# Kernel optimization log

Measured on AMD Instinct MI355X. Metric: run time of the kernel, lower is better.

The kernel has to match this reference:

```python
import jax, jax.numpy as jnp
import numpy as np

B, N_REG, D_IN = 32, 116, 256
N_NODES = B * N_REG            # 3712
E_PER_G = N_REG * 10           # avg degree 10
E = B * E_PER_G                # 37120
HEADS = 8
HID = [256, 128, 64]
D_OUT = 256
LN_EPS = 1e-5


def _layer_norm(x, scale, bias):
    mu = x.mean(-1, keepdims=True)
    var = ((x - mu) ** 2).mean(-1, keepdims=True)
    return (x - mu) * jax.lax.rsqrt(var + LN_EPS) * scale + bias


def _gat_layer(x, W, b, a_src, a_dst, src, dst, concat):
    """PyG-style GATConv (shared lin, self-loops, leaky_relu 0.2) + ELU + LayerNorm."""
    N = x.shape[0]
    H, C = a_src.shape
    h = (x @ W).reshape(N, H, C)                      # (N, H, C)
    sl = jnp.arange(N, dtype=src.dtype)               # self-loops (PyG default)
    s = jnp.concatenate([src, sl])
    d = jnp.concatenate([dst, sl])
    al = (h * a_src).sum(-1)                          # (N, H)
    ar = (h * a_dst).sum(-1)                          # (N, H)
    e = jax.nn.leaky_relu(al[s] + ar[d], 0.2)         # (E', H)
    m = jax.ops.segment_max(e, d, num_segments=N)
    ex = jnp.exp(e - m[d])
    den = jax.ops.segment_sum(ex, d, num_segments=N)
    alpha = ex / den[d]                               # segment softmax over incoming edges
    out = jax.ops.segment_sum(h[s] * alpha[..., None], d, num_segments=N)  # (N, H, C)
    out = out.reshape(N, H * C) if concat else out.mean(1)
    return out + b


def setup_inputs() -> dict:
    key = jax.random.key(0)
    ks = list(jax.random.split(key, 32))
    node_features = jax.random.normal(ks[0], (N_NODES, D_IN), dtype=jnp.float32)
    # edges: random within each graph (disconnected batched graph)
    off = (jnp.arange(B, dtype=jnp.int32) * N_REG)[:, None]
    src = (jax.random.randint(ks[1], (B, E_PER_G), 0, N_REG, dtype=jnp.int32) + off).reshape(-1)
    dst = (jax.random.randint(ks[2], (B, E_PER_G), 0, N_REG, dtype=jnp.int32) + off).reshape(-1)
    batch = jnp.repeat(jnp.arange(B, dtype=jnp.int32), N_REG)

    def lin(k, fin, fout):
        s = 1.0 / np.sqrt(fin)
        return jax.random.uniform(k, (fin, fout), jnp.float32, -s, s)

    dims_in = [D_IN, HID[0] * HEADS, HID[1] * HEADS]
    p = {}
    ki = 3
    for i, (fin, c) in enumerate(zip(dims_in, HID)):
        concat = i < len(HID) - 1
        wdim = c * HEADS
        p[f"w{i}"] = lin(ks[ki], fin, wdim); ki += 1
        p[f"b{i}"] = jnp.zeros((wdim if concat else c,), jnp.float32)
        p[f"as{i}"] = jax.random.normal(ks[ki], (HEADS, c), jnp.float32) * 0.1; ki += 1
        p[f"ad{i}"] = jax.random.normal(ks[ki], (HEADS, c), jnp.float32) * 0.1; ki += 1
        ldim = wdim if concat else c
        p[f"ls{i}"] = jnp.ones((ldim,), jnp.float32)
        p[f"lb{i}"] = jnp.zeros((ldim,), jnp.float32)
    p["wp"] = lin(ks[ki], HID[-1], D_OUT); ki += 1
    p["bp"] = jnp.zeros((D_OUT,), jnp.float32)
    p["lsp"] = jnp.ones((D_OUT,), jnp.float32)
    p["lbp"] = jnp.zeros((D_OUT,), jnp.float32)
    p["wq"] = lin(ks[ki], D_OUT, 1); ki += 1
    p["bq"] = jnp.zeros((1,), jnp.float32)
    return dict(node_features=node_features, src=src, dst=dst, batch=batch, **p)


def reference(node_features, src, dst, batch,
              w0, b0, as0, ad0, ls0, lb0,
              w1, b1, as1, ad1, ls1, lb1,
              w2, b2, as2, ad2, ls2, lb2,
              wp, bp, lsp, lbp, wq, bq):
    x = node_features
    x = _layer_norm(jax.nn.elu(_gat_layer(x, w0, b0, as0, ad0, src, dst, True)), ls0, lb0)
    x = _layer_norm(jax.nn.elu(_gat_layer(x, w1, b1, as1, ad1, src, dst, True)), ls1, lb1)
    x = _layer_norm(jax.nn.elu(_gat_layer(x, w2, b2, as2, ad2, src, dst, False)), ls2, lb2)
    node_out = jax.nn.gelu(_layer_norm(x @ wp + bp, lsp, lbp), approximate=False)  # (N, 256)
    pool_w = jax.nn.softmax(node_out @ wq + bq, axis=0)                            # (N, 1) global softmax
    num = jax.ops.segment_sum(node_out * pool_w, batch, num_segments=B)            # (B, 256)
    den = jnp.maximum(jax.ops.segment_sum(pool_w, batch, num_segments=B), 1e-8)    # (B, 1)
    graph_features = num / den
    return graph_features, node_out
```

## Files before the change

### kernel.cpp

```cpp
#include <hip/hip_runtime.h>
#include <hip/hip_bf16.h>
#include <math.h>

typedef __hip_bfloat16 bf16;
typedef short short8 __attribute__((ext_vector_type(8)));
typedef float f32x4 __attribute__((ext_vector_type(4)));

__device__ __forceinline__ float b2f(const bf16 v) { return __bfloat162float(v); }
__device__ __forceinline__ bf16 f2b(const float v) { return __float2bfloat16(v); }

__device__ __forceinline__ float bits2f(short s) {
  unsigned u = ((unsigned)(unsigned short)s) << 16;
  float f;
  __builtin_memcpy(&f, &u, 4);
  return f;
}
__device__ __forceinline__ short f2bits(float f) {
  bf16 b = f2b(f);
  short s;
  __builtin_memcpy(&s, &b, 2);
  return s;
}

__device__ __forceinline__ float ldsel(const void* p, size_t i, int f32) {
  return f32 ? ((const float*)p)[i] : b2f(((const bf16*)p)[i]);
}
__device__ __forceinline__ void stsel(void* p, size_t i, float v, int f32) {
  if (f32) ((float*)p)[i] = v; else ((bf16*)p)[i] = f2b(v);
}

__device__ __forceinline__ void load8f(const void* p, int idx, int f32, float* o) {
  if (f32) {
    const float4* q = (const float4*)((const float*)p + idx);
    float4 a = q[0], b = q[1];
    o[0] = a.x; o[1] = a.y; o[2] = a.z; o[3] = a.w;
    o[4] = b.x; o[5] = b.y; o[6] = b.z; o[7] = b.w;
  } else {
    union { short8 v; short s[8]; } u;
    u.v = *(const short8*)((const bf16*)p + idx);
#pragma unroll
    for (int j = 0; j < 8; ++j) o[j] = bits2f(u.s[j]);
  }
}

#define NN 3712
#define NE 37120
#define NG 32
#define NREG 116
#define MAXDEG 48


__global__ __launch_bounds__(256) void k_detect(const void* nf, const void* w0, int* flags) {
  __shared__ int bad[2];
  if (threadIdx.x < 2) bad[threadIdx.x] = 0;
  __syncthreads();
  const bf16* a = (const bf16*)nf;
  const bf16* b = (const bf16*)w0;
  int l0 = 0, l1 = 0;
  for (int i = threadIdx.x; i < 4096; i += 256) {
    float x = b2f(a[i]); if (!(fabsf(x) < 1e4f)) l0++;
    float y = b2f(b[i]); if (!(fabsf(y) < 1e4f)) l1++;
  }
  if (l0) atomicAdd(&bad[0], l0);
  if (l1) atomicAdd(&bad[1], l1);
  __syncthreads();
  if (threadIdx.x == 0) { flags[0] = bad[0] > 0; flags[1] = bad[1] > 0; }
}

__global__ __launch_bounds__(256) void k_zero(int* __restrict__ p, int n) {
  int i = blockIdx.x * 256 + threadIdx.x;
  if (i < n) p[i] = 0;
}

__global__ __launch_bounds__(256) void k_scatter(const int* __restrict__ src, const int* __restrict__ dst,
                                                 int* __restrict__ cnt, int* __restrict__ bucket, int E) {
  int e = blockIdx.x * 256 + threadIdx.x;
  if (e < E) {
    int d = dst[e], s = src[e];
    if ((unsigned)d < NN && (unsigned)s < NN) {
      int p = atomicAdd(&cnt[d], 1);
      if (p < MAXDEG) bucket[d * MAXDEG + p] = s;
    }
  }
}

__global__ __launch_bounds__(256) void k_tox0(const void* __restrict__ in, bf16* __restrict__ out,
                                              const int* __restrict__ flags) {
  int f = flags[0];
  int bid = blockIdx.x;
  int n = (bid & 7) * 464 + (bid >> 3);
  int i = n * 256 + threadIdx.x;
  out[i] = f2b(ldsel(in, i, f));
}

__global__ __launch_bounds__(256) void k_transpose(const void* __restrict__ W, bf16* __restrict__ Wt,
                                                   int K, int N, const int* __restrict__ flags) {
  int f = flags[1];
  __shared__ float tile[32][33];
  int tx = threadIdx.x & 31, ty = threadIdx.x >> 5;
  int k0 = blockIdx.x * 32, n0 = blockIdx.y * 32;
#pragma unroll
  for (int i = 0; i < 4; ++i)
    tile[ty + i * 8][tx] = ldsel(W, (size_t)(k0 + ty + i * 8) * N + n0 + tx, f);
  __syncthreads();
#pragma unroll
  for (int i = 0; i < 4; ++i)
    Wt[(size_t)(n0 + ty + i * 8) * K + k0 + tx] = f2b(tile[tx][ty + i * 8]);
}

__global__ __launch_bounds__(256) void k_gemm_mfma(const bf16* __restrict__ A, const bf16* __restrict__ Bt,
                                                   bf16* __restrict__ C, int M, int N, int K) {
  __shared__ short As[64 * 72];
  __shared__ short Bs[64 * 72];
  int tid = threadIdx.x;
  int wave = tid >> 6, lane = tid & 63;
  int wr = wave >> 1, wc = wave & 1;
  int quad = lane >> 4, ml = lane & 15;

  int nbx = N >> 6;
  int total = gridDim.x;
  int id = blockIdx.x;
  int tile = ((total & 7) == 0) ? ((id & 7) * (total >> 3) + (id >> 3)) : id;
  int n0 = (tile % nbx) << 6;
  int m0 = (tile / nbx) << 6;

  f32x4 acc[2][2];
#pragma unroll
  for (int rt = 0; rt < 2; ++rt)
#pragma unroll
    for (int ct = 0; ct < 2; ++ct)
#pragma unroll
      for (int r = 0; r < 4; ++r) acc[rt][ct][r] = 0.f;

  for (int k0 = 0; k0 < K; k0 += 64) {
    __syncthreads();
#pragma unroll
    for (int i = 0; i < 2; ++i) {
      int c = tid + (i << 8);
      int row = c >> 3, kg = (c & 7) << 3;
      *(uint4*)&As[row * 72 + kg] = *(const uint4*)&A[(size_t)(m0 + row) * K + k0 + kg];
      *(uint4*)&Bs[row * 72 + kg] = *(const uint4*)&Bt[(size_t)(n0 + row) * K + k0 + kg];
    }
    __syncthreads();
    short8 af[2][2], bfr[2][2];
#pragma unroll
    for (int rt = 0; rt < 2; ++rt)
#pragma unroll
      for (int kk = 0; kk < 2; ++kk)
        af[rt][kk] = *(const short8*)&As[(wr * 32 + rt * 16 + ml) * 72 + kk * 32 + quad * 8];
#pragma unroll
    for (int ct = 0; ct < 2; ++ct)
#pragma unroll
      for (int kk = 0; kk < 2; ++kk)
        bfr[ct][kk] = *(const short8*)&Bs[(wc * 32 + ct * 16 + ml) * 72 + kk * 32 + quad * 8];
#pragma unroll
    for (int rt = 0; rt < 2; ++rt)
#pragma unroll
      for (int ct = 0; ct < 2; ++ct)
#pragma unroll
        for (int kk = 0; kk < 2; ++kk)
          acc[rt][ct] = __builtin_amdgcn_mfma_f32_16x16x32_bf16(af[rt][kk], bfr[ct][kk], acc[rt][ct], 0, 0, 0);
  }
#pragma unroll
  for (int rt = 0; rt < 2; ++rt)
#pragma unroll
    for (int ct = 0; ct < 2; ++ct)
#pragma unroll
      for (int r = 0; r < 4; ++r) {
        int grow = m0 + wr * 32 + rt * 16 + quad * 4 + r;
        int gcol = n0 + wc * 32 + ct * 16 + ml;
        C[(size_t)grow * N + gcol] = f2b(acc[rt][ct][r]);
      }
}

__global__ void k_attn(const bf16* __restrict__ H, const void* __restrict__ a_s,
                       const void* __restrict__ a_d, float* __restrict__ al,
                       float* __restrict__ ar, int C, const int* __restrict__ flags) {
  int wF = flags[1];
  int t = threadIdx.x;
  int D = 8 * C;
  int i0 = t * 8;
  int bid = blockIdx.x;
  int nb = (bid & 7) * 58 + (bid >> 3);
  float as8[8], ad8[8];
  load8f(a_s, i0, wF, as8);
  load8f(a_d, i0, wF, ad8);
  int G = C >> 3;
  int hd = i0 / C;
  for (int it = 0; it < 8; ++it) {
    int n = nb * 8 + it;
    union { short8 v; short s[8]; } u;
    u.v = *(const short8*)&H[(size_t)n * D + i0];
    float ps = 0.f, pd = 0.f;
#pragma unroll
    for (int j = 0; j < 8; ++j) {
      float h = bits2f(u.s[j]);
      ps = fmaf(h, as8[j], ps);
      pd = fmaf(h, ad8[j], pd);
    }
    for (int off = G >> 1; off; off >>= 1) {
      ps += __shfl_xor(ps, off);
      pd += __shfl_xor(pd, off);
    }
    if ((t & (G - 1)) == 0) {
      al[n * 8 + hd] = ps;
      ar[n * 8 + hd] = pd;
    }
  }
}

__global__ __launch_bounds__(256) void k_edgew(const float* __restrict__ al, const float* __restrict__ ar,
                                               const int* __restrict__ cnt, const int* __restrict__ bucket,
                                               float* __restrict__ mbuf, float* __restrict__ ibuf) {
  int t = threadIdx.x;
  int q = t >> 6, l = t & 63, hd = l >> 3, el = l & 7;
  int bid = blockIdx.x;
  int d = (bid & 7) * 464 + (bid >> 3) * 4 + q;
  int deg = cnt[d]; deg = deg > MAXDEG ? MAXDEG : deg;
  int total = deg + 1;
  float ard = ar[d * 8 + hd];
  float lgv[7];
  float m = -1e30f;
#pragma unroll
  for (int k = 0; k < 7; ++k) {
    int e = el + k * 8;
    float lg = -1e30f;
    if (e < total) {
      int s = e < deg ? bucket[d * MAXDEG + e] : d;
      lg = al[s * 8 + hd] + ard;
      lg = lg > 0.f ? lg : 0.2f * lg;
    }
    lgv[k] = lg;
    m = fmaxf(m, lg);
  }
#pragma unroll
  for (int off = 4; off; off >>= 1) m = fmaxf(m, __shfl_xor(m, off));
  float den = 0.f;
#pragma unroll
  for (int k = 0; k < 7; ++k) den += (lgv[k] > -1e29f) ? expf(lgv[k] - m) : 0.f;
#pragma unroll
  for (int off = 4; off; off >>= 1) den += __shfl_xor(den, off);
  if (el == 0) { mbuf[d * 8 + hd] = m; ibuf[d * 8 + hd] = 1.f / den; }
}

template<int C>
__global__ __launch_bounds__(256, 1) void k_aggm(const bf16* __restrict__ H,
    const float* __restrict__ al, const float* __restrict__ ar,
    const float* __restrict__ mbuf, const float* __restrict__ ibuf,
    const int* __restrict__ cnt, const int* __restrict__ bucket,
    bf16* __restrict__ Y) {
  constexpr int D = 8 * C;
  constexpr int KP = 136;
  __shared__ short P[128 * KP];
  __shared__ short Ht[C * KP];
  int t = threadIdx.x;
  int bid = blockIdx.x;
  int x = bid & 7, j = bid >> 3;
  int g = x * 4 + (j & 3);
  int h = j >> 2;
  int gbase = g * NREG;

  short8 z = {0, 0, 0, 0, 0, 0, 0, 0};
  for (int i = t; i < 128 * KP / 8; i += 256) *(short8*)&P[i * 8] = z;
  for (int i = t; i < C * KP / 8; i += 256) *(short8*)&Ht[i * 8] = z;
  __syncthreads();

  constexpr int CH = C / 8;
  for (int idx = t; idx < NREG * CH; idx += 256) {
    int s = idx / CH, c0 = (idx % CH) * 8;
    union { short8 v; short x2[8]; } u;
    u.v = *(const short8*)&H[(size_t)(gbase + s) * D + h * C + c0];
#pragma unroll
    for (int jj = 0; jj < 8; ++jj) Ht[(c0 + jj) * KP + s] = u.x2[jj];
  }
  if (t < NREG) {
    int gd = gbase + t;
    int deg = cnt[gd]; deg = deg > MAXDEG ? MAXDEG : deg;
    int total = deg + 1;
    float ard = ar[gd * 8 + h];
    float mm = mbuf[gd * 8 + h], inv = ibuf[gd * 8 + h];
    for (int base = 0; base < total; base += 8) {
      int sg[8]; float av[8];
#pragma unroll
      for (int jj = 0; jj < 8; ++jj) {
        int e = base + jj;
        sg[jj] = (e < deg) ? bucket[gd * MAXDEG + e] : gd;
      }
#pragma unroll
      for (int jj = 0; jj < 8; ++jj) av[jj] = al[sg[jj] * 8 + h];
#pragma unroll
      for (int jj = 0; jj < 8; ++jj) {
        if (base + jj < total) {
          float lg = av[jj] + ard;
          lg = lg > 0.f ? lg : 0.2f * lg;
          float alpha = expf(lg - mm) * inv;
          int off = t * KP + (sg[jj] - gbase);
          P[off] = f2bits(bits2f(P[off]) + alpha);
        }
      }
    }
  }
  __syncthreads();

  constexpr int CT = C / 32;
  int wave = t >> 6, lane = t & 63;
  int wr = wave >> 1, wc = wave & 1;
  int quad = lane >> 4, ml = lane & 15;
  f32x4 acc[4][CT];
#pragma unroll
  for (int a = 0; a < 4; ++a)
#pragma unroll
    for (int b = 0; b < CT; ++b)
#pragma unroll
      for (int r = 0; r < 4; ++r) acc[a][b][r] = 0.f;
#pragma unroll
  for (int ks = 0; ks < 4; ++ks) {
    short8 af[4], bf8[CT];
#pragma unroll
    for (int rt = 0; rt < 4; ++rt)
      af[rt] = *(const short8*)&P[(wr * 64 + rt * 16 + ml) * KP + ks * 32 + quad * 8];
#pragma unroll
    for (int ct = 0; ct < CT; ++ct)
      bf8[ct] = *(const short8*)&Ht[(wc * (C / 2) + ct * 16 + ml) * KP + ks * 32 + quad * 8];
#pragma unroll
    for (int rt = 0; rt < 4; ++rt)
#pragma unroll
      for (int ct = 0; ct < CT; ++ct)
        acc[rt][ct] = __builtin_amdgcn_mfma_f32_16x16x32_bf16(af[rt], bf8[ct], acc[rt][ct], 0, 0, 0);
  }
#pragma unroll
  for (int rt = 0; rt < 4; ++rt) {
    int m = wr * 64 + rt * 16 + quad * 4;
#pragma unroll
    for (int r = 0; r < 4; ++r) {
      if (m + r < NREG) {
#pragma unroll
        for (int ct = 0; ct < CT; ++ct) {
          int n = wc * (C / 2) + ct * 16 + ml;
          Y[(size_t)(gbase + m + r) * D + h * C + n] = f2b(acc[rt][ct][r]);
        }
      }
    }
  }
}

template<int D>
__global__ __launch_bounds__(256) void k_ln(bf16* __restrict__ X, const void* __restrict__ bias,
                                            const void* __restrict__ ls, const void* __restrict__ lb,
                                            const int* __restrict__ flags) {
  int wF = flags[1];
  constexpr int VPT = D / 256;
  int t = threadIdx.x;
  int bid = blockIdx.x;
  int nb = (bid & 7) * 58 + (bid >> 3);
  int node = nb * 8 + (t >> 5);
  int l32 = t & 31;
  float v[VPT * 8];
  float s1 = 0.f, s2 = 0.f;
#pragma unroll
  for (int j = 0; j < VPT; ++j) {
    int c0 = (l32 + j * 32) * 8;
    union { short8 u; short x[8]; } uu;
    uu.u = *(const short8*)&X[(size_t)node * D + c0];
    float bb[8];
    load8f(bias, c0, wF, bb);
#pragma unroll
    for (int k = 0; k < 8; ++k) {
      float vv = bits2f(uu.x[k]) + bb[k];
      vv = vv > 0.f ? vv : expf(vv) - 1.f;
      v[j * 8 + k] = vv; s1 += vv; s2 += vv * vv;
    }
  }
#pragma unroll
  for (int off = 16; off; off >>= 1) { s1 += __shfl_xor(s1, off); s2 += __shfl_xor(s2, off); }
  float mu = s1 / D;
  float rs = rsqrtf(s2 / D - mu * mu + 1e-5f);
#pragma unroll
  for (int j = 0; j < VPT; ++j) {
    int c0 = (l32 + j * 32) * 8;
    float g8[8], b8[8];
    load8f(ls, c0, wF, g8);
    load8f(lb, c0, wF, b8);
    union { short8 u; short x[8]; } uu;
#pragma unroll
    for (int k = 0; k < 8; ++k)
      uu.x[k] = f2bits((v[j * 8 + k] - mu) * rs * g8[k] + b8[k]);
    *(short8*)&X[(size_t)node * D + c0] = uu.u;
  }
}

__global__ void k_agg(const bf16* __restrict__ H, const float* __restrict__ al,
                      const float* __restrict__ ar, const float* __restrict__ mbuf,
                      const float* __restrict__ ibuf, const int* __restrict__ cnt,
                      const int* __restrict__ bucket, const void* __restrict__ bias,
                      const void* __restrict__ ls, const void* __restrict__ lb,
                      bf16* __restrict__ Xout, int C, int concat,
                      const int* __restrict__ flags) {
  int wF = flags[1];
  int bid = blockIdx.x;
  int d = (bid & 7) * 464 + (bid >> 3);
  int t = threadIdx.x;
  int D = 8 * C;
  __shared__ int sid[MAXDEG + 4];
  __shared__ float vals[512];

  int deg = cnt[d]; deg = deg > MAXDEG ? MAXDEG : deg;
  int total = deg + 1;
  int padded = (total + 3) & ~3;
  if (t < padded) sid[t] = t < deg ? bucket[d * MAXDEG + t] : d;
  __syncthreads();

  int i0 = t * 8;
  int hd = i0 / C;
  float m = mbuf[d * 8 + hd], inv = ibuf[d * 8 + hd], ard = ar[d * 8 + hd];

  float acc[8] = {0.f, 0.f, 0.f, 0.f, 0.f, 0.f, 0.f, 0.f};
  const bf16* __restrict__ Hp = H + i0;
  for (int eb = 0; eb < padded; eb += 4) {
    int s4[4]; float a4[4]; short8 u4[4];
#pragma unroll
    for (int j = 0; j < 4; ++j) s4[j] = sid[eb + j];
#pragma unroll
    for (int j = 0; j < 4; ++j) {
      a4[j] = al[s4[j] * 8 + hd];
      u4[j] = *(const short8*)&Hp[(size_t)s4[j] * D];
    }
#pragma unroll
    for (int j = 0; j < 4; ++j) {
      float lg = a4[j] + ard;
      lg = lg > 0.f ? lg : 0.2f * lg;
      float we = (eb + j) < total ? expf(lg - m) * inv : 0.f;
      union { short8 v; short s[8]; } uu; uu.v = u4[j];
#pragma unroll
      for (int k2 = 0; k2 < 8; ++k2) acc[k2] = fmaf(we, bits2f(uu.s[k2]), acc[k2]);
    }
  }

#pragma unroll
  for (int j = 0; j < 8; ++j) vals[i0 + j] = acc[j];
  __syncthreads();
  float v = 0.f;
#pragma unroll
  for (int h = 0; h < 8; ++h) v += vals[h * 64 + t];
  v = v * 0.125f + ldsel(bias, t, wF);
  v = v > 0.f ? v : expf(v) - 1.f;
  float s1 = v, s2 = v * v;
#pragma unroll
  for (int off = 32; off; off >>= 1) { s1 += __shfl_xor(s1, off); s2 += __shfl_xor(s2, off); }
  float mu = s1 * (1.f / 64.f);
  float var = s2 * (1.f / 64.f) - mu * mu;
  float rs = rsqrtf(var + 1e-5f);
  Xout[(size_t)d * 64 + t] = f2b((v - mu) * rs * ldsel(ls, t, wF) + ldsel(lb, t, wF));
}

__global__ __launch_bounds__(256) void k_proj(const bf16* __restrict__ X3, const void* __restrict__ wp,
                                              const void* __restrict__ bp, const void* __restrict__ lsp,
                                              const void* __restrict__ lbp, const void* __restrict__ wq,
                                              const void* __restrict__ bq,
                                              float* __restrict__ q, void* __restrict__ dout,
                                              const int* __restrict__ flags) {
  int wF = flags[1], xF = flags[0];
  int bid = blockIdx.x;
  int n = (bid & 7) * 464 + (bid >> 3);
  int t = threadIdx.x;
  int lane = t & 63, wave = t >> 6;
  __shared__ float xs[64];
  __shared__ float r1[4], r2[4];
  __shared__ float sMu, sRs;
  if (t < 64) xs[t] = b2f(X3[n * 64 + t]);
  __syncthreads();
  float y = ldsel(bp, t, wF);
#pragma unroll 8
  for (int k = 0; k < 64; ++k) y = fmaf(xs[k], ldsel(wp, k * 256 + t, wF), y);
  float s1 = y, s2 = y * y;
#pragma unroll
  for (int off = 32; off; off >>= 1) { s1 += __shfl_down(s1, off); s2 += __shfl_down(s2, off); }
  if (lane == 0) { r1[wave] = s1; r2[wave] = s2; }
  __syncthreads();
  if (t == 0) {
    float S1 = r1[0] + r1[1] + r1[2] + r1[3];
    float S2 = r2[0] + r2[1] + r2[2] + r2[3];
    float mu = S1 / 256.f;
    sMu = mu; sRs = rsqrtf(S2 / 256.f - mu * mu + 1e-5f);
  }
  __syncthreads();
  float v = (y - sMu) * sRs * ldsel(lsp, t, wF) + ldsel(lbp, t, wF);
  float g = 0.5f * v * (1.f + erff(v * 0.70710678118654752f));
  stsel(dout, (size_t)NG * 256 + (size_t)n * 256 + t, g, xF);
  float qv = g * ldsel(wq, t, wF);
#pragma unroll
  for (int off = 32; off; off >>= 1) qv += __shfl_down(qv, off);
  if (lane == 0) r1[wave] = qv;
  __syncthreads();
  if (t == 0) q[n] = r1[0] + r1[1] + r1[2] + r1[3] + ldsel(bq, 0, wF);
}

__global__ __launch_bounds__(256) void k_pool(void* __restrict__ dout, const float* __restrict__ q,
                                              const int* __restrict__ flags) {
  int xF = flags[0];
  int bid = blockIdx.x;
  int b = (bid & 7) * 4 + (bid >> 3);
  int t = threadIdx.x;
  __shared__ float es[NREG];
  __shared__ float sDen;
  if (t < NREG) es[t] = q[b * NREG + t];
  __syncthreads();
  if (t == 0) {
    float m = -1e30f;
    for (int i = 0; i < NREG; ++i) m = fmaxf(m, es[i]);
    float den = 0.f;
    for (int i = 0; i < NREG; ++i) { float e = expf(es[i] - m); es[i] = e; den += e; }
    sDen = den;
  }
  __syncthreads();
  float acc = 0.f;
  for (int i = 0; i < NREG; ++i)
    acc = fmaf(es[i], ldsel(dout, (size_t)NG * 256 + (size_t)(b * NREG + i) * 256 + t, xF), acc);
  stsel(dout, (size_t)b * 256 + t, acc / sDen, xF);
}

extern "C" void kernel_launch(void* const* d_in, const int* in_sizes, int n_in,
                              void* d_out, int out_size, void* d_ws, size_t ws_size,
                              hipStream_t stream) {
  const void* nf  = d_in[0];
  const int* src  = (const int*)d_in[1];
  const int* dst  = (const int*)d_in[2];
  const void *w0 = d_in[4],  *b0 = d_in[5],  *as0 = d_in[6], *ad0 = d_in[7],  *ls0 = d_in[8],  *lb0 = d_in[9];
  const void *w1 = d_in[10], *b1 = d_in[11], *as1 = d_in[12], *ad1 = d_in[13], *ls1 = d_in[14], *lb1 = d_in[15];
  const void *w2 = d_in[16], *b2 = d_in[17], *as2 = d_in[18], *ad2 = d_in[19], *ls2 = d_in[20], *lb2 = d_in[21];
  const void *wp = d_in[22], *bp = d_in[23], *lsp = d_in[24], *lbp = d_in[25], *wq = d_in[26], *bq = d_in[27];

  int* flags  = (int*)d_ws;
  float* al   = (float*)(flags + 4);
  float* ar   = al + NN * 8;
  int* cnt    = (int*)(ar + NN * 8);
  int* bucket = cnt + NN;
  float* q    = (float*)(bucket + NN * MAXDEG);
  bf16* X     = (bf16*)(q + NN);
  bf16* Hb    = X + (size_t)NN * 2048;

  float* mbuf = (float*)d_out;
  float* ibuf = mbuf + NN * 8;

  bf16* X0  = X;
  bf16* wt0 = X + (1 << 20);
  bf16* wt1 = Hb + (size_t)NN * 1024;
  bf16* wt2 = Hb + (size_t)NN * 512;

  k_detect<<<1, 256, 0, stream>>>(nf, w0, flags);
  k_zero<<<(NN + 255) / 256, 256, 0, stream>>>(cnt, NN);
  k_scatter<<<(NE + 255) / 256, 256, 0, stream>>>(src, dst, cnt, bucket, NE);
  k_tox0<<<NN, 256, 0, stream>>>(nf, X0, flags);

  k_transpose<<<dim3(256 / 32, 2048 / 32), 256, 0, stream>>>(w0, wt0, 256, 2048, flags);
  k_gemm_mfma<<<(2048 / 64) * (NN / 64), 256, 0, stream>>>(X0, wt0, Hb, NN, 2048, 256);
  k_attn<<<NN / 8, 256, 0, stream>>>(Hb, as0, ad0, al, ar, 256, flags);
  k_edgew<<<NN / 4, 256, 0, stream>>>(al, ar, cnt, bucket, mbuf, ibuf);
  k_aggm<256><<<256, 256, 0, stream>>>(Hb, al, ar, mbuf, ibuf, cnt, bucket, X);
  k_ln<2048><<<NN / 8, 256, 0, stream>>>(X, b0, ls0, lb0, flags);

  k_transpose<<<dim3(2048 / 32, 1024 / 32), 256, 0, stream>>>(w1, wt1, 2048, 1024, flags);
  k_gemm_mfma<<<(1024 / 64) * (NN / 64), 256, 0, stream>>>(X, wt1, Hb, NN, 1024, 2048);
  k_attn<<<NN / 8, 128, 0, stream>>>(Hb, as1, ad1, al, ar, 128, flags);
  k_edgew<<<NN / 4, 256, 0, stream>>>(al, ar, cnt, bucket, mbuf, ibuf);
  k_aggm<128><<<256, 256, 0, stream>>>(Hb, al, ar, mbuf, ibuf, cnt, bucket, X);
  k_ln<1024><<<NN / 8, 256, 0, stream>>>(X, b1, ls1, lb1, flags);

  k_transpose<<<dim3(1024 / 32, 512 / 32), 256, 0, stream>>>(w2, wt2, 1024, 512, flags);
  k_gemm_mfma<<<(512 / 64) * (NN / 64), 256, 0, stream>>>(X, wt2, Hb, NN, 512, 1024);
  k_attn<<<NN / 8, 64, 0, stream>>>(Hb, as2, ad2, al, ar, 64, flags);
  k_edgew<<<NN / 4, 256, 0, stream>>>(al, ar, cnt, bucket, mbuf, ibuf);
  k_agg<<<NN, 64, 0, stream>>>(Hb, al, ar, mbuf, ibuf, cnt, bucket, b2, ls2, lb2, X, 64, 0, flags);

  k_proj<<<NN, 256, 0, stream>>>(X, wp, bp, lsp, lbp, wq, bq, q, d_out, flags);
  k_pool<<<NG, 256, 0, stream>>>(d_out, q, flags);
}
```

Measured before the change: 335.4 us.

## Fuse attention logits and edge softmax into per-graph aggregation kernel

Removes the separate k_attn and k_edgew kernels. The per-node source and destination attention logits are now computed inside k_aggm while H is staged into shared memory, using shared-memory atomics, and the per-destination softmax max and denominator are computed in-block from shared memory. The last layer now also uses the MFMA k_aggm<64> path followed by a new mean+ELU+LayerNorm kernel instead of the gather-based k_agg. This saves launches and global round-trips for al/ar/m/inv, in exchange for three serial passes over edges per thread and LDS atomic contention.

Result: slower. 356.1 us (+6.2%).

```diff
diff --git a/kernel.cpp b/kernel.cpp
--- a/kernel.cpp
+++ b/kernel.cpp
@@ -173,86 +173,17 @@
       }
 }
 
-__global__ void k_attn(const bf16* __restrict__ H, const void* __restrict__ a_s,
-                       const void* __restrict__ a_d, float* __restrict__ al,
-                       float* __restrict__ ar, int C, const int* __restrict__ flags) {
-  int wF = flags[1];
-  int t = threadIdx.x;
-  int D = 8 * C;
-  int i0 = t * 8;
-  int bid = blockIdx.x;
-  int nb = (bid & 7) * 58 + (bid >> 3);
-  float as8[8], ad8[8];
-  load8f(a_s, i0, wF, as8);
-  load8f(a_d, i0, wF, ad8);
-  int G = C >> 3;
-  int hd = i0 / C;
-  for (int it = 0; it < 8; ++it) {
-    int n = nb * 8 + it;
-    union { short8 v; short s[8]; } u;
-    u.v = *(const short8*)&H[(size_t)n * D + i0];
-    float ps = 0.f, pd = 0.f;
-#pragma unroll
-    for (int j = 0; j < 8; ++j) {
-      float h = bits2f(u.s[j]);
-      ps = fmaf(h, as8[j], ps);
-      pd = fmaf(h, ad8[j], pd);
-    }
-    for (int off = G >> 1; off; off >>= 1) {
-      ps += __shfl_xor(ps, off);
-      pd += __shfl_xor(pd, off);
-    }
-    if ((t & (G - 1)) == 0) {
-      al[n * 8 + hd] = ps;
-      ar[n * 8 + hd] = pd;
-    }
-  }
-}
-
-__global__ __launch_bounds__(256) void k_edgew(const float* __restrict__ al, const float* __restrict__ ar,
-                                               const int* __restrict__ cnt, const int* __restrict__ bucket,
-                                               float* __restrict__ mbuf, float* __restrict__ ibuf) {
-  int t = threadIdx.x;
-  int q = t >> 6, l = t & 63, hd = l >> 3, el = l & 7;
-  int bid = blockIdx.x;
-  int d = (bid & 7) * 464 + (bid >> 3) * 4 + q;
-  int deg = cnt[d]; deg = deg > MAXDEG ? MAXDEG : deg;
-  int total = deg + 1;
-  float ard = ar[d * 8 + hd];
-  float lgv[7];
-  float m = -1e30f;
-#pragma unroll
-  for (int k = 0; k < 7; ++k) {
-    int e = el + k * 8;
-    float lg = -1e30f;
-    if (e < total) {
-      int s = e < deg ? bucket[d * MAXDEG + e] : d;
-      lg = al[s * 8 + hd] + ard;
-      lg = lg > 0.f ? lg : 0.2f * lg;
-    }
-    lgv[k] = lg;
-    m = fmaxf(m, lg);
-  }
-#pragma unroll
-  for (int off = 4; off; off >>= 1) m = fmaxf(m, __shfl_xor(m, off));
-  float den = 0.f;
-#pragma unroll
-  for (int k = 0; k < 7; ++k) den += (lgv[k] > -1e29f) ? expf(lgv[k] - m) : 0.f;
-#pragma unroll
-  for (int off = 4; off; off >>= 1) den += __shfl_xor(den, off);
-  if (el == 0) { mbuf[d * 8 + hd] = m; ibuf[d * 8 + hd] = 1.f / den; }
-}
-
 template<int C>
 __global__ __launch_bounds__(256, 1) void k_aggm(const bf16* __restrict__ H,
-    const float* __restrict__ al, const float* __restrict__ ar,
-    const float* __restrict__ mbuf, const float* __restrict__ ibuf,
+    const void* __restrict__ a_s, const void* __restrict__ a_d,
     const int* __restrict__ cnt, const int* __restrict__ bucket,
-    bf16* __restrict__ Y) {
+    bf16* __restrict__ Y, const int* __restrict__ flags) {
   constexpr int D = 8 * C;
   constexpr int KP = 136;
   __shared__ short P[128 * KP];
   __shared__ short Ht[C * KP];
+  __shared__ float alS[128], arS[128];
+  int wF = flags[1];
   int t = threadIdx.x;
   int bid = blockIdx.x;
   int x = bid & 7, j = bid >> 3;
@@ -263,6 +194,7 @@
   short8 z = {0, 0, 0, 0, 0, 0, 0, 0};
   for (int i = t; i < 128 * KP / 8; i += 256) *(short8*)&P[i * 8] = z;
   for (int i = t; i < C * KP / 8; i += 256) *(short8*)&Ht[i * 8] = z;
+  if (t < 128) { alS[t] = 0.f; arS[t] = 0.f; }
   __syncthreads();
 
   constexpr int CH = C / 8;
@@ -270,34 +202,49 @@
     int s = idx / CH, c0 = (idx % CH) * 8;
     union { short8 v; short x2[8]; } u;
     u.v = *(const short8*)&H[(size_t)(gbase + s) * D + h * C + c0];
-#pragma unroll
-    for (int jj = 0; jj < 8; ++jj) Ht[(c0 + jj) * KP + s] = u.x2[jj];
-  }
+    float as8[8], ad8[8];
+    load8f(a_s, h * C + c0, wF, as8);
+    load8f(a_d, h * C + c0, wF, ad8);
+    float ps = 0.f, pd = 0.f;
+#pragma unroll
+    for (int jj = 0; jj < 8; ++jj) {
+      float hv = bits2f(u.x2[jj]);
+      Ht[(c0 + jj) * KP + s] = u.x2[jj];
+      ps = fmaf(hv, as8[jj], ps);
+      pd = fmaf(hv, ad8[jj], pd);
+    }
+    atomicAdd(&alS[s], ps);
+    atomicAdd(&arS[s], pd);
+  }
+  __syncthreads();
+
   if (t < NREG) {
     int gd = gbase + t;
     int deg = cnt[gd]; deg = deg > MAXDEG ? MAXDEG : deg;
     int total = deg + 1;
-    float ard = ar[gd * 8 + h];
-    float mm = mbuf[gd * 8 + h], inv = ibuf[gd * 8 + h];
-    for (int base = 0; base < total; base += 8) {
-      int sg[8]; float av[8];
-#pragma unroll
-      for (int jj = 0; jj < 8; ++jj) {
-        int e = base + jj;
-        sg[jj] = (e < deg) ? bucket[gd * MAXDEG + e] : gd;
-      }
-#pragma unroll
-      for (int jj = 0; jj < 8; ++jj) av[jj] = al[sg[jj] * 8 + h];
-#pragma unroll
-      for (int jj = 0; jj < 8; ++jj) {
-        if (base + jj < total) {
-          float lg = av[jj] + ard;
-          lg = lg > 0.f ? lg : 0.2f * lg;
-          float alpha = expf(lg - mm) * inv;
-          int off = t * KP + (sg[jj] - gbase);
-          P[off] = f2bits(bits2f(P[off]) + alpha);
-        }
-      }
+    float ard = arS[t];
+    float m = -1e30f;
+    for (int e = 0; e < total; ++e) {
+      int s = e < deg ? bucket[gd * MAXDEG + e] - gbase : t;
+      float lg = alS[s] + ard;
+      lg = lg > 0.f ? lg : 0.2f * lg;
+      m = fmaxf(m, lg);
+    }
+    float den = 0.f;
+    for (int e = 0; e < total; ++e) {
+      int s = e < deg ? bucket[gd * MAXDEG + e] - gbase : t;
+      float lg = alS[s] + ard;
+      lg = lg > 0.f ? lg : 0.2f * lg;
+      den += expf(lg - m);
+    }
+    float inv = 1.f / den;
+    for (int e = 0; e < total; ++e) {
+      int s = e < deg ? bucket[gd * MAXDEG + e] - gbase : t;
+      float lg = alS[s] + ard;
+      lg = lg > 0.f ? lg : 0.2f * lg;
+      float alpha = expf(lg - m) * inv;
+      int off = t * KP + s;
+      P[off] = f2bits(bits2f(P[off]) + alpha);
     }
   }
   __syncthreads();
@@ -330,14 +277,14 @@
   }
 #pragma unroll
   for (int rt = 0; rt < 4; ++rt) {
-    int m = wr * 64 + rt * 16 + quad * 4;
+    int m2 = wr * 64 + rt * 16 + quad * 4;
 #pragma unroll
     for (int r = 0; r < 4; ++r) {
-      if (m + r < NREG) {
+      if (m2 + r < NREG) {
 #pragma unroll
         for (int ct = 0; ct < CT; ++ct) {
           int n = wc * (C / 2) + ct * 16 + ml;
-          Y[(size_t)(gbase + m + r) * D + h * C + n] = f2b(acc[rt][ct][r]);
+          Y[(size_t)(gbase + m2 + r) * D + h * C + n] = f2b(acc[rt][ct][r]);
         }
       }
     }
@@ -389,68 +336,25 @@
   }
 }
 
-__global__ void k_agg(const bf16* __restrict__ H, const float* __restrict__ al,
-                      const float* __restrict__ ar, const float* __restrict__ mbuf,
-                      const float* __restrict__ ibuf, const int* __restrict__ cnt,
-                      const int* __restrict__ bucket, const void* __restrict__ bias,
-                      const void* __restrict__ ls, const void* __restrict__ lb,
-                      bf16* __restrict__ Xout, int C, int concat,
-                      const int* __restrict__ flags) {
+__global__ __launch_bounds__(256) void k_lnmean(const bf16* __restrict__ Yr, bf16* __restrict__ X3,
+                                                const void* __restrict__ bias, const void* __restrict__ ls,
+                                                const void* __restrict__ lb, const int* __restrict__ flags) {
   int wF = flags[1];
-  int bid = blockIdx.x;
-  int d = (bid & 7) * 464 + (bid >> 3);
   int t = threadIdx.x;
-  int D = 8 * C;
-  __shared__ int sid[MAXDEG + 4];
-  __shared__ float vals[512];
-
-  int deg = cnt[d]; deg = deg > MAXDEG ? MAXDEG : deg;
-  int total = deg + 1;
-  int padded = (total + 3) & ~3;
-  if (t < padded) sid[t] = t < deg ? bucket[d * MAXDEG + t] : d;
-  __syncthreads();
-
-  int i0 = t * 8;
-  int hd = i0 / C;
-  float m = mbuf[d * 8 + hd], inv = ibuf[d * 8 + hd], ard = ar[d * 8 + hd];
-
-  float acc[8] = {0.f, 0.f, 0.f, 0.f, 0.f, 0.f, 0.f, 0.f};
-  const bf16* __restrict__ Hp = H + i0;
-  for (int eb = 0; eb < padded; eb += 4) {
-    int s4[4]; float a4[4]; short8 u4[4];
-#pragma unroll
-    for (int j = 0; j < 4; ++j) s4[j] = sid[eb + j];
-#pragma unroll
-    for (int j = 0; j < 4; ++j) {
-      a4[j] = al[s4[j] * 8 + hd];
-      u4[j] = *(const short8*)&Hp[(size_t)s4[j] * D];
-    }
-#pragma unroll
-    for (int j = 0; j < 4; ++j) {
-      float lg = a4[j] + ard;
-      lg = lg > 0.f ? lg : 0.2f * lg;
-      float we = (eb + j) < total ? expf(lg - m) * inv : 0.f;
-      union { short8 v; short s[8]; } uu; uu.v = u4[j];
-#pragma unroll
-      for (int k2 = 0; k2 < 8; ++k2) acc[k2] = fmaf(we, bits2f(uu.s[k2]), acc[k2]);
-    }
-  }
-
-#pragma unroll
-  for (int j = 0; j < 8; ++j) vals[i0 + j] = acc[j];
-  __syncthreads();
+  int bid = blockIdx.x;
+  int q = t >> 6, l = t & 63;
+  int n = (bid & 7) * 464 + (bid >> 3) * 4 + q;
   float v = 0.f;
 #pragma unroll
-  for (int h = 0; h < 8; ++h) v += vals[h * 64 + t];
-  v = v * 0.125f + ldsel(bias, t, wF);
+  for (int h = 0; h < 8; ++h) v += b2f(Yr[(size_t)n * 512 + h * 64 + l]);
+  v = v * 0.125f + ldsel(bias, l, wF);
   v = v > 0.f ? v : expf(v) - 1.f;
   float s1 = v, s2 = v * v;
 #pragma unroll
   for (int off = 32; off; off >>= 1) { s1 += __shfl_xor(s1, off); s2 += __shfl_xor(s2, off); }
   float mu = s1 * (1.f / 64.f);
-  float var = s2 * (1.f / 64.f) - mu * mu;
-  float rs = rsqrtf(var + 1e-5f);
-  Xout[(size_t)d * 64 + t] = f2b((v - mu) * rs * ldsel(ls, t, wF) + ldsel(lb, t, wF));
+  float rs = rsqrtf(s2 * (1.f / 64.f) - mu * mu + 1e-5f);
+  X3[(size_t)n * 64 + l] = f2b((v - mu) * rs * ldsel(ls, l, wF) + ldsel(lb, l, wF));
 }
 
 __global__ __launch_bounds__(256) void k_proj(const bf16* __restrict__ X3, const void* __restrict__ wp,
@@ -538,14 +442,13 @@
   float* q    = (float*)(bucket + NN * MAXDEG);
   bf16* X     = (bf16*)(q + NN);
   bf16* Hb    = X + (size_t)NN * 2048;
-
-  float* mbuf = (float*)d_out;
-  float* ibuf = mbuf + NN * 8;
+  (void)al; (void)ar;
 
   bf16* X0  = X;
   bf16* wt0 = X + (1 << 20);
   bf16* wt1 = Hb + (size_t)NN * 1024;
   bf16* wt2 = Hb + (size_t)NN * 512;
+  bf16* X3  = X + (size_t)NN * 512;
 
   k_detect<<<1, 256, 0, stream>>>(nf, w0, flags);
   k_zero<<<(NN + 255) / 256, 256, 0, stream>>>(cnt, NN);
@@ -554,24 +457,19 @@
 
   k_transpose<<<dim3(256 / 32, 2048 / 32), 256, 0, stream>>>(w0, wt0, 256, 2048, flags);
   k_gemm_mfma<<<(2048 / 64) * (NN / 64), 256, 0, stream>>>(X0, wt0, Hb, NN, 2048, 256);
-  k_attn<<<NN / 8, 256, 0, stream>>>(Hb, as0, ad0, al, ar, 256, flags);
-  k_edgew<<<NN / 4, 256, 0, stream>>>(al, ar, cnt, bucket, mbuf, ibuf);
-  k_aggm<256><<<256, 256, 0, stream>>>(Hb, al, ar, mbuf, ibuf, cnt, bucket, X);
+  k_aggm<256><<<256, 256, 0, stream>>>(Hb, as0, ad0, cnt, bucket, X, flags);
   k_ln<2048><<<NN / 8, 256, 0, stream>>>(X, b0, ls0, lb0, flags);
 
   k_transpose<<<dim3(2048 / 32, 1024 / 32), 256, 0, stream>>>(w1, wt1, 2048, 1024, flags);
   k_gemm_mfma<<<(1024 / 64) * (NN / 64), 256, 0, stream>>>(X, wt1, Hb, NN, 1024, 2048);
-  k_attn<<<NN / 8, 128, 0, stream>>>(Hb, as1, ad1, al, ar, 128, flags);
-  k_edgew<<<NN / 4, 256, 0, stream>>>(al, ar, cnt, bucket, mbuf, ibuf);
-  k_aggm<128><<<256, 256, 0, stream>>>(Hb, al, ar, mbuf, ibuf, cnt, bucket, X);
+  k_aggm<128><<<256, 256, 0, stream>>>(Hb, as1, ad1, cnt, bucket, X, flags);
   k_ln<1024><<<NN / 8, 256, 0, stream>>>(X, b1, ls1, lb1, flags);
 
   k_transpose<<<dim3(1024 / 32, 512 / 32), 256, 0, stream>>>(w2, wt2, 1024, 512, flags);
   k_gemm_mfma<<<(512 / 64) * (NN / 64), 256, 0, stream>>>(X, wt2, Hb, NN, 512, 1024);
-  k_attn<<<NN / 8, 64, 0, stream>>>(Hb, as2, ad2, al, ar, 64, flags);
-  k_edgew<<<NN / 4, 256, 0, stream>>>(al, ar, cnt, bucket, mbuf, ibuf);
-  k_agg<<<NN, 64, 0, stream>>>(Hb, al, ar, mbuf, ibuf, cnt, bucket, b2, ls2, lb2, X, 64, 0, flags);
-
-  k_proj<<<NN, 256, 0, stream>>>(X, wp, bp, lsp, lbp, wq, bq, q, d_out, flags);
+  k_aggm<64><<<256, 256, 0, stream>>>(Hb, as2, ad2, cnt, bucket, X, flags);
+  k_lnmean<<<NN / 4, 256, 0, stream>>>(X, X3, b2, ls2, lb2, flags);
+
+  k_proj<<<NN, 256, 0, stream>>>(X3, wp, bp, lsp, lbp, wq, bq, q, d_out, flags);
   k_pool<<<NG, 256, 0, stream>>>(d_out, q, flags);
 }
```
